# Performance work log

Hardware: AMD Instinct MI355X
Metric: run time of the kernel (lower is better)

Reference implementation:

```python
import jax, jax.numpy as jnp
import numpy as np

B = 32768   # batch (agents)
D = 2       # data_dim
E = 16      # embedding_dim
H = 128     # h_dim
M = 6       # num_modes
T = 30      # pred_len
EPS = 1e-5  # GroupNorm eps


def gn(x, w, b):
    # GroupNorm with 1 group over the last (channel) axis, per sample
    mu = x.mean(-1, keepdims=True)
    var = x.var(-1, keepdims=True)
    return (x - mu) * jax.lax.rsqrt(var + EPS) * w + b


def setup_inputs() -> dict:
    key = jax.random.key(0)
    ks = jax.random.split(key, 24)
    def n(k, shp, s=0.08):
        return jax.random.normal(k, shp, jnp.float32) * s
    return dict(
        last_obs=jax.random.normal(ks[0], (B, D), jnp.float32),
        last_obs_rel=jax.random.normal(ks[1], (B, D), jnp.float32),
        h0=jax.random.normal(ks[2], (B, H), jnp.float32),
        c0=jax.random.normal(ks[3], (B, H), jnp.float32),
        W_se=n(ks[4], (E, M * D)), b_se=n(ks[5], (E,)),
        W_ih=n(ks[6], (4 * H, E)), W_hh=n(ks[7], (4 * H, H)),
        b_ih=n(ks[8], (4 * H,)), b_hh=n(ks[9], (4 * H,)),
        mW1=n(ks[10], (M, H, H)), mg1w=jnp.ones((M, H)), mg1b=jnp.zeros((M, H)),
        mW2=n(ks[11], (M, H, H)), mg2w=jnp.ones((M, H)), mg2b=jnp.zeros((M, H)),
        mWo=n(ks[12], (M, H, D)), mbo=n(ks[13], (M, D)),
        cW1=n(ks[14], (H, H)), cg1w=jnp.ones((H,)), cg1b=jnp.zeros((H,)),
        cW2=n(ks[15], (H, H)), cg2w=jnp.ones((H,)), cg2b=jnp.zeros((H,)),
        cWo=n(ks[16], (H, M)), cbo=n(ks[17], (M,)),
    )


def reference(last_obs, last_obs_rel, h0, c0, W_se, b_se, W_ih, W_hh, b_ih, b_hh,
              mW1, mg1w, mg1b, mW2, mg2w, mg2b, mWo, mbo,
              cW1, cg1w, cg1b, cW2, cg2w, cg2b, cWo, cbo):
    assert last_obs.shape[1] == D
    # initial decoder input: last_obs_rel repeated over modes -> (B, M*D)
    x0 = jnp.tile(last_obs_rel, (1, M))
    dec_in = jax.nn.selu(x0 @ W_se.T + b_se)  # (B, E)

    def mode_heads(h):
        # six LinearRes(H,H,GN ng=1)+Linear(H,D) heads, batched over mode axis m
        t = jnp.einsum('bd,mde->mbe', h, mW1)
        t = jax.nn.relu(gn(t, mg1w[:, None, :], mg1b[:, None, :]))
        t = jnp.einsum('mbe,mef->mbf', t, mW2)
        t = gn(t, mg2w[:, None, :], mg2b[:, None, :])
        t = jax.nn.relu(t + h[None])
        out = jnp.einsum('mbf,mfo->mbo', t, mWo) + mbo[:, None, :]  # (M,B,D)
        return jnp.swapaxes(out, 0, 1)  # (B,M,D) -- cat over modes layout

    def step(carry, _):
        h, c, xin = carry
        g = xin @ W_ih.T + b_ih + h @ W_hh.T + b_hh  # (B, 4H), torch gate order i,f,g,o
        i, f, gg, o = jnp.split(g, 4, axis=-1)
        c = jax.nn.sigmoid(f) * c + jax.nn.sigmoid(i) * jnp.tanh(gg)
        h = jax.nn.sigmoid(o) * jnp.tanh(c)
        rel = mode_heads(h)  # (B,M,D)
        xin = jax.nn.selu(rel.reshape(rel.shape[0], M * D) @ W_se.T + b_se)
        return (h, c, xin), rel

    (hT, cT, _), rels = jax.lax.scan(step, (h0, c0, dec_in), None, length=T)
    pred = jnp.transpose(rels, (1, 2, 0, 3))  # (B, M, T, D)

    # confidence head: LinearRes + Linear(H, M) + softmax
    t = jax.nn.relu(gn(hT @ cW1, cg1w, cg1b))
    t = gn(t @ cW2, cg2w, cg2b)
    t = jax.nn.relu(t + hT)
    conf = jax.nn.softmax(t @ cWo + cbo, axis=1)  # (B, M)
    return pred, conf
```

## Files before the change

### kernel.cpp

```cpp
#include <hip/hip_runtime.h>
#include <hip/hip_bf16.h>
#include <cstdint>
#include <cstddef>


#define HD 128
#define TT 30
#define MM 6
#define B_ROWS 32768

typedef _Float16 f16x8 __attribute__((ext_vector_type(8)));
typedef _Float16 f16x4 __attribute__((ext_vector_type(4)));
typedef float f32x4 __attribute__((ext_vector_type(4)));

__device__ __forceinline__ float fast_rcp(float x) { return __builtin_amdgcn_rcpf(x); }
__device__ __forceinline__ float sigm(float x) { return fast_rcp(1.f + __expf(-x)); }
__device__ __forceinline__ float tanhf_(float x) { return 1.f - 2.f * fast_rcp(__expf(2.f * x) + 1.f); }
__device__ __forceinline__ float selu_(float x) {
  const float sc = 1.0507009873554805f;
  const float al = 1.6732632423543772f;
  return x > 0.f ? sc * x : sc * al * (__expf(x) - 1.f);
}

__device__ __forceinline__ f32x4 shx4(f32x4 v, int m) {
  f32x4 r;
  r[0] = __shfl_xor(v[0], m, 64);
  r[1] = __shfl_xor(v[1], m, 64);
  r[2] = __shfl_xor(v[2], m, 64);
  r[3] = __shfl_xor(v[3], m, 64);
  return r;
}

__global__ __launch_bounds__(256) void prep_weights(
    const float* __restrict__ W_ih, const float* __restrict__ W_hh,
    const float* __restrict__ b_ih, const float* __restrict__ b_hh,
    const float* __restrict__ mW1, const float* __restrict__ mW2,
    const float* __restrict__ cW1, const float* __restrict__ cW2,
    _Float16* __restrict__ Wg, _Float16* __restrict__ W1p, _Float16* __restrict__ W2p,
    _Float16* __restrict__ cW1p, _Float16* __restrict__ cW2p, float* __restrict__ bg) {
  int n = blockIdx.x * 256 + threadIdx.x;
  if (n < 81920) {
    int t16 = n / 2560, r = n % 2560;
    int ch = r / 512, l = (r >> 3) & 63, j = r & 7;
    int q = l >> 4, cl = l & 15;
    int cg = t16 >> 2, g = t16 & 3;
    int row = g * 128 + cg * 16 + cl;
    int k = ch * 32 + q * 8 + j;
    float v = 0.f;
    if (k < 128) v = W_hh[row * 128 + k];
    else if (k < 144) v = W_ih[row * 16 + (k - 128)];
    Wg[n] = (_Float16)v;
    return;
  }
  n -= 81920;
  if (n < 98304) {
    int m = n >> 14, r = n & 16383;
    int ct = r >> 11, ch = (r >> 9) & 3, l = (r >> 3) & 63, j = r & 7;
    int q = l >> 4, cl = l & 15;
    int outcol = ct * 16 + cl, k = ch * 32 + q * 8 + j;
    W1p[n] = (_Float16)mW1[(m * 128 + k) * 128 + outcol];
    return;
  }
  n -= 98304;
  if (n < 98304) {
    int m = n >> 14, r = n & 16383;
    int ct = r >> 11, ch = (r >> 9) & 3, l = (r >> 3) & 63, j = r & 7;
    int q = l >> 4, cl = l & 15;
    int outcol = ct * 16 + cl, k = ch * 32 + q * 8 + j;
    W2p[n] = (_Float16)mW2[(m * 128 + k) * 128 + outcol];
    return;
  }
  n -= 98304;
  if (n < 16384) {
    int ct = n >> 11, ch = (n >> 9) & 3, l = (n >> 3) & 63, j = n & 7;
    int q = l >> 4, cl = l & 15;
    int outcol = ct * 16 + cl, k = ch * 32 + q * 8 + j;
    cW1p[n] = (_Float16)cW1[k * 128 + outcol];
    return;
  }
  n -= 16384;
  if (n < 16384) {
    int ct = n >> 11, ch = (n >> 9) & 3, l = (n >> 3) & 63, j = n & 7;
    int q = l >> 4, cl = l & 15;
    int outcol = ct * 16 + cl, k = ch * 32 + q * 8 + j;
    cW2p[n] = (_Float16)cW2[k * 128 + outcol];
    return;
  }
  n -= 16384;
  if (n < 512) bg[n] = b_ih[n] + b_hh[n];
}

__device__ __forceinline__ void stage_chunk(int idx, _Float16* dst, int w, int lane,
                                            const _Float16* __restrict__ Wg,
                                            const _Float16* __restrict__ W1p,
                                            const _Float16* __restrict__ W2p) {
  const _Float16* src;
  int nblk;
  if (idx < 8) {
    src = Wg + idx * 10240;
    nblk = 20;
  } else {
    int j = idx - 8, m = j >> 2, r = j & 3;
    src = ((r & 2) ? W2p : W1p) + m * 16384 + (r & 1) * 8192;
    nblk = 16;
  }
  for (int i = w; i < nblk; i += 4) {
    __builtin_amdgcn_global_load_lds(
        (const __attribute__((address_space(1))) void*)(src + i * 512 + lane * 8),
        (__attribute__((address_space(3))) void*)(dst + i * 512 + lane * 8),
        16, 0, 0);
  }
}

__device__ __forceinline__ f32x4 mfma16(f16x8 a, f16x8 b, f32x4 c) {
  return __builtin_amdgcn_mfma_f32_16x16x32_f16(a, b, c, 0, 0, 0);
}

__device__ __forceinline__ void gemm_half(const f16x8 (&a)[4], const _Float16* buf,
                                          int lane, f32x4 (&acc)[8], int base) {
#pragma unroll
  for (int ctl = 0; ctl < 4; ++ctl) {
    const _Float16* bp = buf + ctl * 2048 + lane * 8;
    f32x4 a0 = {0.f, 0.f, 0.f, 0.f};
#pragma unroll
    for (int ch = 0; ch < 4; ++ch) {
      f16x8 b = *(const f16x8*)(bp + ch * 512);
      a0 = mfma16(a[ch], b, a0);
    }
    acc[base + ctl] = a0;
  }
}

__global__ __launch_bounds__(256, 2) void mmdec_main(
    const float* __restrict__ last_obs_rel, const float* __restrict__ h0, const float* __restrict__ c0,
    const float* __restrict__ W_se, const float* __restrict__ b_se,
    const float* __restrict__ mg1w, const float* __restrict__ mg1b,
    const float* __restrict__ mg2w, const float* __restrict__ mg2b,
    const float* __restrict__ mWo, const float* __restrict__ mbo,
    const float* __restrict__ cg1w, const float* __restrict__ cg1b,
    const float* __restrict__ cg2w, const float* __restrict__ cg2b,
    const float* __restrict__ cWo, const float* __restrict__ cbo,
    const _Float16* __restrict__ Wg, const _Float16* __restrict__ W1p, const _Float16* __restrict__ W2p,
    const _Float16* __restrict__ cW1p, const _Float16* __restrict__ cW2p, const float* __restrict__ bgp,
    float* __restrict__ out) {
  __shared__ __align__(16) unsigned char smem[81920];
  _Float16* stage0 = (_Float16*)smem;
  unsigned char* h_base = smem + 40960;
  unsigned char* t1_base = smem + 61440;
  float* rel_all = (float*)(smem + 78848);

  const int tid = threadIdx.x;
  const int w = tid >> 6;
  const int lane = tid & 63;
  const int q = lane >> 4, cl = lane & 15;
  const int rowbase = blockIdx.x * 64 + w * 16;

  auto hrow = [&](int r) -> _Float16* { return (_Float16*)(h_base + (w * 16 + r) * 320); };
  auto t1row = [&](int r) -> _Float16* { return (_Float16*)(t1_base + (w * 16 + r) * 272); };
  float* relw = rel_all + w * 16 * 12;

  auto sbuf = [&](int idx) -> _Float16* { return stage0 + ((idx & 1) ? 10240 : 0); };

  {
    const int rr = lane & 15, seg = lane >> 4;
    const float* src = h0 + (size_t)(rowbase + rr) * HD + seg * 32;
    _Float16* dst = hrow(rr) + seg * 32;
#pragma unroll
    for (int i = 0; i < 32; i += 8) {
      f16x8 v;
#pragma unroll
      for (int k = 0; k < 8; ++k) v[k] = (_Float16)src[i + k];
      *(f16x8*)(dst + i) = v;
    }
    const float r0 = last_obs_rel[(size_t)(rowbase + rr) * 2 + 0];
    const float r1 = last_obs_rel[(size_t)(rowbase + rr) * 2 + 1];
    const int e0 = seg * 4;
    f16x4 v;
#pragma unroll
    for (int i = 0; i < 4; ++i) {
      const int e = e0 + i;
      float acc = b_se[e];
#pragma unroll
      for (int j = 0; j < 12; ++j) acc += ((j & 1) ? r1 : r0) * W_se[e * 12 + j];
      v[i] = (_Float16)selu_(acc);
    }
    *(f16x4*)(hrow(rr) + 128 + e0) = v;
    if (lane < 16) {
      f16x8 z;
#pragma unroll
      for (int i = 0; i < 8; ++i) z[i] = (_Float16)0.f;
      *(f16x8*)(hrow(lane) + 144) = z;
      *(f16x8*)(hrow(lane) + 152) = z;
    }
  }
  f32x4 cacc[8];
#pragma unroll
  for (int cg = 0; cg < 8; ++cg)
#pragma unroll
    for (int r = 0; r < 4; ++r)
      cacc[cg][r] = c0[(size_t)(rowbase + q * 4 + r) * HD + cg * 16 + cl];
  float bgh[8][4];
#pragma unroll
  for (int cg = 0; cg < 8; ++cg)
#pragma unroll
    for (int g = 0; g < 4; ++g) bgh[cg][g] = bgp[g * 128 + cg * 16 + cl];
  f32x4 hc[8];

  stage_chunk(0, sbuf(0), w, lane, Wg, W1p, W2p);
  __syncthreads();

  const size_t confbase = (size_t)B_ROWS * MM * TT * 2;

  for (int t = 0; t < TT; ++t) {
    f16x8 afr[5];
#pragma unroll
    for (int ch = 0; ch < 5; ++ch)
      afr[ch] = *(const f16x8*)(hrow(cl) + ch * 32 + q * 8);

    for (int cg = 0; cg < 8; ++cg) {
      stage_chunk((cg + 1) & 31, sbuf(cg + 1), w, lane, Wg, W1p, W2p);
      const _Float16* buf = sbuf(cg);
      f32x4 gacc[4];
#pragma unroll
      for (int g = 0; g < 4; ++g) gacc[g] = f32x4{0.f, 0.f, 0.f, 0.f};
#pragma unroll
      for (int g = 0; g < 4; ++g) {
        const _Float16* bp = buf + g * 2560 + lane * 8;
#pragma unroll
        for (int ch = 0; ch < 5; ++ch) {
          f16x8 b = *(const f16x8*)(bp + ch * 512);
          gacc[g] = mfma16(afr[ch], b, gacc[g]);
        }
      }
#pragma unroll
      for (int r = 0; r < 4; ++r) {
        const float iv = sigm(gacc[0][r] + bgh[cg][0]);
        const float fv = sigm(gacc[1][r] + bgh[cg][1]);
        const float gv = tanhf_(gacc[2][r] + bgh[cg][2]);
        const float ov = sigm(gacc[3][r] + bgh[cg][3]);
        const float cn = fv * cacc[cg][r] + iv * gv;
        cacc[cg][r] = cn;
        const float hv = ov * tanhf_(cn);
        hc[cg][r] = hv;
        hrow(q * 4 + r)[cg * 16 + cl] = (_Float16)hv;
      }
      __syncthreads();
    }

    f16x8 frag[4];
#pragma unroll
    for (int ch = 0; ch < 4; ++ch)
      frag[ch] = *(const f16x8*)(hrow(cl) + ch * 32 + q * 8);

    for (int m = 0; m < MM; ++m) {
      const int base = 8 + m * 4;

      f32x4 acc1[8];
      stage_chunk((base + 1) & 31, sbuf(base + 1), w, lane, Wg, W1p, W2p);
      gemm_half(frag, sbuf(base), lane, acc1, 0);
      __syncthreads();
      stage_chunk((base + 2) & 31, sbuf(base + 2), w, lane, Wg, W1p, W2p);
      gemm_half(frag, sbuf(base + 1), lane, acc1, 4);
      f32x4 mean, rstd;
      {
        f32x4 s1 = {0.f, 0.f, 0.f, 0.f}, s2 = {0.f, 0.f, 0.f, 0.f};
#pragma unroll
        for (int ct = 0; ct < 8; ++ct) { s1 += acc1[ct]; s2 += acc1[ct] * acc1[ct]; }
#pragma unroll
        for (int sh = 1; sh < 16; sh <<= 1) { s1 += shx4(s1, sh); s2 += shx4(s2, sh); }
        mean = s1 * (1.f / 128.f);
#pragma unroll
        for (int r = 0; r < 4; ++r)
          rstd[r] = rsqrtf(s2[r] * (1.f / 128.f) - mean[r] * mean[r] + 1e-5f);
      }
#pragma unroll
      for (int ct = 0; ct < 8; ++ct) {
        const float g1 = mg1w[m * HD + ct * 16 + cl];
        const float b1 = mg1b[m * HD + ct * 16 + cl];
#pragma unroll
        for (int r = 0; r < 4; ++r) {
          float v = (acc1[ct][r] - mean[r]) * rstd[r] * g1 + b1;
          t1row(q * 4 + r)[ct * 16 + cl] = (_Float16)fmaxf(v, 0.f);
        }
      }
      __syncthreads();
      f16x8 at1[4];
#pragma unroll
      for (int ch = 0; ch < 4; ++ch)
        at1[ch] = *(const f16x8*)(t1row(cl) + ch * 32 + q * 8);
      f32x4 acc2[8];
      stage_chunk((base + 3) & 31, sbuf(base + 3), w, lane, Wg, W1p, W2p);
      gemm_half(at1, sbuf(base + 2), lane, acc2, 0);
      __syncthreads();
      stage_chunk((base + 4) & 31, sbuf(base + 4), w, lane, Wg, W1p, W2p);
      gemm_half(at1, sbuf(base + 3), lane, acc2, 4);
      f32x4 mean2, rstd2;
      {
        f32x4 s1 = {0.f, 0.f, 0.f, 0.f}, s2 = {0.f, 0.f, 0.f, 0.f};
#pragma unroll
        for (int ct = 0; ct < 8; ++ct) { s1 += acc2[ct]; s2 += acc2[ct] * acc2[ct]; }
#pragma unroll
        for (int sh = 1; sh < 16; sh <<= 1) { s1 += shx4(s1, sh); s2 += shx4(s2, sh); }
        mean2 = s1 * (1.f / 128.f);
#pragma unroll
        for (int r = 0; r < 4; ++r)
          rstd2[r] = rsqrtf(s2[r] * (1.f / 128.f) - mean2[r] * mean2[r] + 1e-5f);
      }
      f32x4 po0 = {0.f, 0.f, 0.f, 0.f}, po1 = {0.f, 0.f, 0.f, 0.f};
#pragma unroll
      for (int ct = 0; ct < 8; ++ct) {
        const float g2 = mg2w[m * HD + ct * 16 + cl];
        const float b2 = mg2b[m * HD + ct * 16 + cl];
        const float w0 = mWo[((size_t)m * HD + ct * 16 + cl) * 2 + 0];
        const float w1 = mWo[((size_t)m * HD + ct * 16 + cl) * 2 + 1];
#pragma unroll
        for (int r = 0; r < 4; ++r) {
          float v = (acc2[ct][r] - mean2[r]) * rstd2[r] * g2 + b2 + hc[ct][r];
          v = fmaxf(v, 0.f);
          po0[r] += v * w0;
          po1[r] += v * w1;
        }
      }
#pragma unroll
      for (int sh = 1; sh < 16; sh <<= 1) { po0 += shx4(po0, sh); po1 += shx4(po1, sh); }
      if (cl < 2) {
#pragma unroll
        for (int r = 0; r < 4; ++r) {
          const int rl_ = q * 4 + r;
          const float val = (cl ? po1[r] : po0[r]) + mbo[m * 2 + cl];
          out[(((size_t)(rowbase + rl_) * MM + m) * TT + t) * 2 + cl] = val;
          relw[rl_ * 12 + m * 2 + cl] = val;
        }
      }
      __syncthreads();
    }

    {
      const int rr = lane & 15, e0 = (lane >> 4) * 4;
      float rl[12];
#pragma unroll
      for (int j = 0; j < 12; ++j) rl[j] = relw[rr * 12 + j];
      f16x4 v;
#pragma unroll
      for (int i = 0; i < 4; ++i) {
        const int e = e0 + i;
        float acc = b_se[e];
#pragma unroll
        for (int j = 0; j < 12; ++j) acc += rl[j] * W_se[e * 12 + j];
        v[i] = (_Float16)selu_(acc);
      }
      *(f16x4*)(hrow(rr) + 128 + e0) = v;
    }
  }

  {
    f16x8 frag[4];
#pragma unroll
    for (int ch = 0; ch < 4; ++ch)
      frag[ch] = *(const f16x8*)(hrow(cl) + ch * 32 + q * 8);
    f32x4 acc1[8];
#pragma unroll
    for (int ct = 0; ct < 8; ++ct) {
      const _Float16* bp = cW1p + ct * 2048 + lane * 8;
      f32x4 a0 = {0.f, 0.f, 0.f, 0.f};
#pragma unroll
      for (int ch = 0; ch < 4; ++ch) {
        f16x8 b = *(const f16x8*)(bp + ch * 512);
        a0 = mfma16(frag[ch], b, a0);
      }
      acc1[ct] = a0;
    }
    f32x4 mean, rstd;
    {
      f32x4 s1 = {0.f, 0.f, 0.f, 0.f}, s2 = {0.f, 0.f, 0.f, 0.f};
#pragma unroll
      for (int ct = 0; ct < 8; ++ct) { s1 += acc1[ct]; s2 += acc1[ct] * acc1[ct]; }
#pragma unroll
      for (int sh = 1; sh < 16; sh <<= 1) { s1 += shx4(s1, sh); s2 += shx4(s2, sh); }
      mean = s1 * (1.f / 128.f);
#pragma unroll
      for (int r = 0; r < 4; ++r)
        rstd[r] = rsqrtf(s2[r] * (1.f / 128.f) - mean[r] * mean[r] + 1e-5f);
    }
#pragma unroll
    for (int ct = 0; ct < 8; ++ct) {
      const float g1 = cg1w[ct * 16 + cl];
      const float b1 = cg1b[ct * 16 + cl];
#pragma unroll
      for (int r = 0; r < 4; ++r) {
        float v = (acc1[ct][r] - mean[r]) * rstd[r] * g1 + b1;
        t1row(q * 4 + r)[ct * 16 + cl] = (_Float16)fmaxf(v, 0.f);
      }
    }
    f16x8 at1[4];
#pragma unroll
    for (int ch = 0; ch < 4; ++ch)
      at1[ch] = *(const f16x8*)(t1row(cl) + ch * 32 + q * 8);
    f32x4 acc2[8];
#pragma unroll
    for (int ct = 0; ct < 8; ++ct) {
      const _Float16* bp = cW2p + ct * 2048 + lane * 8;
      f32x4 a0 = {0.f, 0.f, 0.f, 0.f};
#pragma unroll
      for (int ch = 0; ch < 4; ++ch) {
        f16x8 b = *(const f16x8*)(bp + ch * 512);
        a0 = mfma16(at1[ch], b, a0);
      }
      acc2[ct] = a0;
    }
    f32x4 mean2, rstd2;
    {
      f32x4 s1 = {0.f, 0.f, 0.f, 0.f}, s2 = {0.f, 0.f, 0.f, 0.f};
#pragma unroll
      for (int ct = 0; ct < 8; ++ct) { s1 += acc2[ct]; s2 += acc2[ct] * acc2[ct]; }
#pragma unroll
      for (int sh = 1; sh < 16; sh <<= 1) { s1 += shx4(s1, sh); s2 += shx4(s2, sh); }
      mean2 = s1 * (1.f / 128.f);
#pragma unroll
      for (int r = 0; r < 4; ++r)
        rstd2[r] = rsqrtf(s2[r] * (1.f / 128.f) - mean2[r] * mean2[r] + 1e-5f);
    }
    float pl[4][6];
#pragma unroll
    for (int r = 0; r < 4; ++r)
#pragma unroll
      for (int k = 0; k < 6; ++k) pl[r][k] = 0.f;
#pragma unroll
    for (int ct = 0; ct < 8; ++ct) {
      const float g2 = cg2w[ct * 16 + cl];
      const float b2 = cg2b[ct * 16 + cl];
      float wo[6];
#pragma unroll
      for (int k = 0; k < 6; ++k) wo[k] = cWo[(ct * 16 + cl) * 6 + k];
#pragma unroll
      for (int r = 0; r < 4; ++r) {
        float v = (acc2[ct][r] - mean2[r]) * rstd2[r] * g2 + b2 + hc[ct][r];
        v = fmaxf(v, 0.f);
#pragma unroll
        for (int k = 0; k < 6; ++k) pl[r][k] += v * wo[k];
      }
    }
#pragma unroll
    for (int sh = 1; sh < 16; sh <<= 1)
#pragma unroll
      for (int r = 0; r < 4; ++r)
#pragma unroll
        for (int k = 0; k < 6; ++k) pl[r][k] += __shfl_xor(pl[r][k], sh, 64);
    if (cl == 0) {
#pragma unroll
      for (int r = 0; r < 4; ++r) {
        float l[6];
#pragma unroll
        for (int k = 0; k < 6; ++k) l[k] = pl[r][k] + cbo[k];
        float mx = l[0];
#pragma unroll
        for (int k = 1; k < 6; ++k) mx = fmaxf(mx, l[k]);
        float s = 0.f;
#pragma unroll
        for (int k = 0; k < 6; ++k) { l[k] = __expf(l[k] - mx); s += l[k]; }
        const float inv = fast_rcp(s);
#pragma unroll
        for (int k = 0; k < 6; ++k)
          out[confbase + (size_t)(rowbase + q * 4 + r) * 6 + k] = l[k] * inv;
      }
    }
  }
}

extern "C" void kernel_launch(void* const* d_in, const int* in_sizes, int n_in,
                              void* d_out, int out_size, void* d_ws, size_t ws_size,
                              hipStream_t stream) {
  (void)in_sizes; (void)n_in; (void)out_size; (void)ws_size;
  const float* last_obs_rel = (const float*)d_in[1];
  const float* h0   = (const float*)d_in[2];
  const float* c0   = (const float*)d_in[3];
  const float* W_se = (const float*)d_in[4];
  const float* b_se = (const float*)d_in[5];
  const float* W_ih = (const float*)d_in[6];
  const float* W_hh = (const float*)d_in[7];
  const float* b_ih = (const float*)d_in[8];
  const float* b_hh = (const float*)d_in[9];
  const float* mW1  = (const float*)d_in[10];
  const float* mg1w = (const float*)d_in[11];
  const float* mg1b = (const float*)d_in[12];
  const float* mW2  = (const float*)d_in[13];
  const float* mg2w = (const float*)d_in[14];
  const float* mg2b = (const float*)d_in[15];
  const float* mWo  = (const float*)d_in[16];
  const float* mbo  = (const float*)d_in[17];
  const float* cW1  = (const float*)d_in[18];
  const float* cg1w = (const float*)d_in[19];
  const float* cg1b = (const float*)d_in[20];
  const float* cW2  = (const float*)d_in[21];
  const float* cg2w = (const float*)d_in[22];
  const float* cg2b = (const float*)d_in[23];
  const float* cWo  = (const float*)d_in[24];
  const float* cbo  = (const float*)d_in[25];

  char* ws = (char*)d_ws;
  _Float16* Wg   = (_Float16*)(ws + 0);
  _Float16* W1p  = (_Float16*)(ws + 163840);
  _Float16* W2p  = (_Float16*)(ws + 360448);
  _Float16* cW1p = (_Float16*)(ws + 557056);
  _Float16* cW2p = (_Float16*)(ws + 589824);
  float*    bg   = (float*)   (ws + 622592);

  prep_weights<<<1218, 256, 0, stream>>>(W_ih, W_hh, b_ih, b_hh, mW1, mW2, cW1, cW2,
                                         Wg, W1p, W2p, cW1p, cW2p, bg);
  mmdec_main<<<B_ROWS / 64, 256, 0, stream>>>(last_obs_rel, h0, c0, W_se, b_se,
                                              mg1w, mg1b, mg2w, mg2b, mWo, mbo,
                                              cg1w, cg1b, cg2w, cg2b, cWo, cbo,
                                              Wg, W1p, W2p, cW1p, cW2p, bg, (float*)d_out);
}
```

Baseline: 1.937 ms.

## Give each wave private double-buffered weight staging and use DPP row reductions

Workgroup-wide weight staging with __syncthreads is replaced by per-wave private double buffers. Each wave loads its own copy of every weight tile through global_load_lds in finer per-tile steps and waits with explicit vmcnt and lgkmcnt counters, so all block barriers in the time loop go away. Cross-lane shuffle reductions over 16 lanes become DPP row_shr adds. The trade is that each wave now fetches the full weights itself, roughly four times the L2 traffic, in smaller chunks. The tight counter-based waits also make the result depend on the exact number of memory operations in flight.

Result: slower. 3.366 ms (+73.8%).

```diff
diff --git a/kernel.cpp b/kernel.cpp
--- a/kernel.cpp
+++ b/kernel.cpp
@@ -22,13 +22,24 @@
   return x > 0.f ? sc * x : sc * al * (__expf(x) - 1.f);
 }
 
-__device__ __forceinline__ f32x4 shx4(f32x4 v, int m) {
-  f32x4 r;
-  r[0] = __shfl_xor(v[0], m, 64);
-  r[1] = __shfl_xor(v[1], m, 64);
-  r[2] = __shfl_xor(v[2], m, 64);
-  r[3] = __shfl_xor(v[3], m, 64);
-  return r;
+template <int CTRL>
+__device__ __forceinline__ float dpp_add(float x) {
+  union { float f; int i; } a, b;
+  a.f = x;
+  b.i = __builtin_amdgcn_update_dpp(a.i, a.i, CTRL, 0xF, 0xF, false);
+  return x + b.f;
+}
+__device__ __forceinline__ float rowsum16(float x) {
+  x = dpp_add<0x128>(x);
+  x = dpp_add<0x124>(x);
+  x = dpp_add<0x122>(x);
+  x = dpp_add<0x121>(x);
+  return x;
+}
+__device__ __forceinline__ f32x4 rowsum16x4(f32x4 v) {
+  v[0] = rowsum16(v[0]); v[1] = rowsum16(v[1]);
+  v[2] = rowsum16(v[2]); v[3] = rowsum16(v[3]);
+  return v;
 }
 
 __global__ __launch_bounds__(256) void prep_weights(
@@ -90,45 +101,8 @@
   if (n < 512) bg[n] = b_ih[n] + b_hh[n];
 }
 
-__device__ __forceinline__ void stage_chunk(int idx, _Float16* dst, int w, int lane,
-                                            const _Float16* __restrict__ Wg,
-                                            const _Float16* __restrict__ W1p,
-                                            const _Float16* __restrict__ W2p) {
-  const _Float16* src;
-  int nblk;
-  if (idx < 8) {
-    src = Wg + idx * 10240;
-    nblk = 20;
-  } else {
-    int j = idx - 8, m = j >> 2, r = j & 3;
-    src = ((r & 2) ? W2p : W1p) + m * 16384 + (r & 1) * 8192;
-    nblk = 16;
-  }
-  for (int i = w; i < nblk; i += 4) {
-    __builtin_amdgcn_global_load_lds(
-        (const __attribute__((address_space(1))) void*)(src + i * 512 + lane * 8),
-        (__attribute__((address_space(3))) void*)(dst + i * 512 + lane * 8),
-        16, 0, 0);
-  }
-}
-
 __device__ __forceinline__ f32x4 mfma16(f16x8 a, f16x8 b, f32x4 c) {
   return __builtin_amdgcn_mfma_f32_16x16x32_f16(a, b, c, 0, 0, 0);
-}
-
-__device__ __forceinline__ void gemm_half(const f16x8 (&a)[4], const _Float16* buf,
-                                          int lane, f32x4 (&acc)[8], int base) {
-#pragma unroll
-  for (int ctl = 0; ctl < 4; ++ctl) {
-    const _Float16* bp = buf + ctl * 2048 + lane * 8;
-    f32x4 a0 = {0.f, 0.f, 0.f, 0.f};
-#pragma unroll
-    for (int ch = 0; ch < 4; ++ch) {
-      f16x8 b = *(const f16x8*)(bp + ch * 512);
-      a0 = mfma16(a[ch], b, a0);
-    }
-    acc[base + ctl] = a0;
-  }
 }
 
 __global__ __launch_bounds__(256, 2) void mmdec_main(
@@ -155,11 +129,17 @@
   const int q = lane >> 4, cl = lane & 15;
   const int rowbase = blockIdx.x * 64 + w * 16;
 
+  _Float16* stg = stage0 + w * 5120;
+
   auto hrow = [&](int r) -> _Float16* { return (_Float16*)(h_base + (w * 16 + r) * 320); };
   auto t1row = [&](int r) -> _Float16* { return (_Float16*)(t1_base + (w * 16 + r) * 272); };
   float* relw = rel_all + w * 16 * 12;
 
-  auto sbuf = [&](int idx) -> _Float16* { return stage0 + ((idx & 1) ? 10240 : 0); };
+  auto gll = [&](const _Float16* s, _Float16* d) {
+    __builtin_amdgcn_global_load_lds(
+        (const __attribute__((address_space(1))) void*)s,
+        (__attribute__((address_space(3))) void*)d, 16, 0, 0);
+  };
 
   {
     const int rr = lane & 15, seg = lane >> 4;
@@ -206,31 +186,55 @@
     for (int g = 0; g < 4; ++g) bgh[cg][g] = bgp[g * 128 + cg * 16 + cl];
   f32x4 hc[8];
 
-  stage_chunk(0, sbuf(0), w, lane, Wg, W1p, W2p);
-  __syncthreads();
+#pragma unroll
+  for (int i = 0; i < 5; ++i) gll(Wg + i * 512 + lane * 8, stg + i * 512 + lane * 8);
+  int cur = 0;
 
   const size_t confbase = (size_t)B_ROWS * MM * TT * 2;
 
   for (int t = 0; t < TT; ++t) {
+    const bool strict = (t == 0);
+    int u = 0;
+    auto advance = [&](int nu) {
+      _Float16* dd = stg + ((cur ^ 1) ? 2560 : 0);
+      asm volatile("s_waitcnt lgkmcnt(0)" ::: "memory");
+      __builtin_amdgcn_sched_barrier(0);
+      if (nu < 32) {
+        const _Float16* src = Wg + nu * 2560;
+#pragma unroll
+        for (int i = 0; i < 5; ++i) gll(src + i * 512 + lane * 8, dd + i * 512 + lane * 8);
+        if (strict) asm volatile("s_waitcnt vmcnt(0)" ::: "memory");
+        else        asm volatile("s_waitcnt vmcnt(5)" ::: "memory");
+      } else {
+        const int j = nu - 32, mm = j >> 4, k = j & 15;
+        const _Float16* src = ((k & 8) ? W2p : W1p) + mm * 16384 + (k & 7) * 2048;
+#pragma unroll
+        for (int i = 0; i < 4; ++i) gll(src + i * 512 + lane * 8, dd + i * 512 + lane * 8);
+        if (strict) asm volatile("s_waitcnt vmcnt(0)" ::: "memory");
+        else        asm volatile("s_waitcnt vmcnt(4)" ::: "memory");
+      }
+      __builtin_amdgcn_sched_barrier(0);
+    };
+
     f16x8 afr[5];
 #pragma unroll
     for (int ch = 0; ch < 5; ++ch)
       afr[ch] = *(const f16x8*)(hrow(cl) + ch * 32 + q * 8);
 
     for (int cg = 0; cg < 8; ++cg) {
-      stage_chunk((cg + 1) & 31, sbuf(cg + 1), w, lane, Wg, W1p, W2p);
-      const _Float16* buf = sbuf(cg);
       f32x4 gacc[4];
 #pragma unroll
-      for (int g = 0; g < 4; ++g) gacc[g] = f32x4{0.f, 0.f, 0.f, 0.f};
-#pragma unroll
       for (int g = 0; g < 4; ++g) {
-        const _Float16* bp = buf + g * 2560 + lane * 8;
+        advance((u + 1) & 127);
+        const _Float16* bp = stg + (cur ? 2560 : 0) + lane * 8;
+        f32x4 a = {0.f, 0.f, 0.f, 0.f};
 #pragma unroll
         for (int ch = 0; ch < 5; ++ch) {
           f16x8 b = *(const f16x8*)(bp + ch * 512);
-          gacc[g] = mfma16(afr[ch], b, gacc[g]);
+          a = mfma16(afr[ch], b, a);
         }
+        gacc[g] = a;
+        cur ^= 1; ++u;
       }
 #pragma unroll
       for (int r = 0; r < 4; ++r) {
@@ -244,7 +248,6 @@
         hc[cg][r] = hv;
         hrow(q * 4 + r)[cg * 16 + cl] = (_Float16)hv;
       }
-      __syncthreads();
     }
 
     f16x8 frag[4];
@@ -253,21 +256,26 @@
       frag[ch] = *(const f16x8*)(hrow(cl) + ch * 32 + q * 8);
 
     for (int m = 0; m < MM; ++m) {
-      const int base = 8 + m * 4;
-
       f32x4 acc1[8];
-      stage_chunk((base + 1) & 31, sbuf(base + 1), w, lane, Wg, W1p, W2p);
-      gemm_half(frag, sbuf(base), lane, acc1, 0);
-      __syncthreads();
-      stage_chunk((base + 2) & 31, sbuf(base + 2), w, lane, Wg, W1p, W2p);
-      gemm_half(frag, sbuf(base + 1), lane, acc1, 4);
+#pragma unroll
+      for (int ct = 0; ct < 8; ++ct) {
+        advance((u + 1) & 127);
+        const _Float16* bp = stg + (cur ? 2560 : 0) + lane * 8;
+        f32x4 a = {0.f, 0.f, 0.f, 0.f};
+#pragma unroll
+        for (int ch = 0; ch < 4; ++ch) {
+          f16x8 b = *(const f16x8*)(bp + ch * 512);
+          a = mfma16(frag[ch], b, a);
+        }
+        acc1[ct] = a;
+        cur ^= 1; ++u;
+      }
       f32x4 mean, rstd;
       {
         f32x4 s1 = {0.f, 0.f, 0.f, 0.f}, s2 = {0.f, 0.f, 0.f, 0.f};
 #pragma unroll
         for (int ct = 0; ct < 8; ++ct) { s1 += acc1[ct]; s2 += acc1[ct] * acc1[ct]; }
-#pragma unroll
-        for (int sh = 1; sh < 16; sh <<= 1) { s1 += shx4(s1, sh); s2 += shx4(s2, sh); }
+        s1 = rowsum16x4(s1); s2 = rowsum16x4(s2);
         mean = s1 * (1.f / 128.f);
 #pragma unroll
         for (int r = 0; r < 4; ++r)
@@ -283,24 +291,30 @@
           t1row(q * 4 + r)[ct * 16 + cl] = (_Float16)fmaxf(v, 0.f);
         }
       }
-      __syncthreads();
       f16x8 at1[4];
 #pragma unroll
       for (int ch = 0; ch < 4; ++ch)
         at1[ch] = *(const f16x8*)(t1row(cl) + ch * 32 + q * 8);
       f32x4 acc2[8];
-      stage_chunk((base + 3) & 31, sbuf(base + 3), w, lane, Wg, W1p, W2p);
-      gemm_half(at1, sbuf(base + 2), lane, acc2, 0);
-      __syncthreads();
-      stage_chunk((base + 4) & 31, sbuf(base + 4), w, lane, Wg, W1p, W2p);
-      gemm_half(at1, sbuf(base + 3), lane, acc2, 4);
+#pragma unroll
+      for (int ct = 0; ct < 8; ++ct) {
+        advance((u + 1) & 127);
+        const _Float16* bp = stg + (cur ? 2560 : 0) + lane * 8;
+        f32x4 a = {0.f, 0.f, 0.f, 0.f};
+#pragma unroll
+        for (int ch = 0; ch < 4; ++ch) {
+          f16x8 b = *(const f16x8*)(bp + ch * 512);
+          a = mfma16(at1[ch], b, a);
+        }
+        acc2[ct] = a;
+        cur ^= 1; ++u;
+      }
       f32x4 mean2, rstd2;
       {
         f32x4 s1 = {0.f, 0.f, 0.f, 0.f}, s2 = {0.f, 0.f, 0.f, 0.f};
 #pragma unroll
         for (int ct = 0; ct < 8; ++ct) { s1 += acc2[ct]; s2 += acc2[ct] * acc2[ct]; }
-#pragma unroll
-        for (int sh = 1; sh < 16; sh <<= 1) { s1 += shx4(s1, sh); s2 += shx4(s2, sh); }
+        s1 = rowsum16x4(s1); s2 = rowsum16x4(s2);
         mean2 = s1 * (1.f / 128.f);
 #pragma unroll
         for (int r = 0; r < 4; ++r)
@@ -321,8 +335,8 @@
           po1[r] += v * w1;
         }
       }
-#pragma unroll
-      for (int sh = 1; sh < 16; sh <<= 1) { po0 += shx4(po0, sh); po1 += shx4(po1, sh); }
+      po0 = rowsum16x4(po0);
+      po1 = rowsum16x4(po1);
       if (cl < 2) {
 #pragma unroll
         for (int r = 0; r < 4; ++r) {
@@ -332,7 +346,6 @@
           relw[rl_ * 12 + m * 2 + cl] = val;
         }
       }
-      __syncthreads();
     }
 
     {
@@ -375,8 +388,7 @@
       f32x4 s1 = {0.f, 0.f, 0.f, 0.f}, s2 = {0.f, 0.f, 0.f, 0.f};
 #pragma unroll
       for (int ct = 0; ct < 8; ++ct) { s1 += acc1[ct]; s2 += acc1[ct] * acc1[ct]; }
-#pragma unroll
-      for (int sh = 1; sh < 16; sh <<= 1) { s1 += shx4(s1, sh); s2 += shx4(s2, sh); }
+      s1 = rowsum16x4(s1); s2 = rowsum16x4(s2);
       mean = s1 * (1.f / 128.f);
 #pragma unroll
       for (int r = 0; r < 4; ++r)
@@ -413,8 +425,7 @@
       f32x4 s1 = {0.f, 0.f, 0.f, 0.f}, s2 = {0.f, 0.f, 0.f, 0.f};
 #pragma unroll
       for (int ct = 0; ct < 8; ++ct) { s1 += acc2[ct]; s2 += acc2[ct] * acc2[ct]; }
-#pragma unroll
-      for (int sh = 1; sh < 16; sh <<= 1) { s1 += shx4(s1, sh); s2 += shx4(s2, sh); }
+      s1 = rowsum16x4(s1); s2 = rowsum16x4(s2);
       mean2 = s1 * (1.f / 128.f);
 #pragma unroll
       for (int r = 0; r < 4; ++r)
@@ -441,11 +452,9 @@
       }
     }
 #pragma unroll
-    for (int sh = 1; sh < 16; sh <<= 1)
-#pragma unroll
-      for (int r = 0; r < 4; ++r)
-#pragma unroll
-        for (int k = 0; k < 6; ++k) pl[r][k] += __shfl_xor(pl[r][k], sh, 64);
+    for (int r = 0; r < 4; ++r)
+#pragma unroll
+      for (int k = 0; k < 6; ++k) pl[r][k] = rowsum16(pl[r][k]);
     if (cl == 0) {
 #pragma unroll
       for (int r = 0; r < 4; ++r) {
```
